# Kernel tuning notes

Hardware: AMD Instinct MI355X
Metric: run time of the kernel (lower is better)

The kernel has to match this reference:

```python
import jax, jax.numpy as jnp
import numpy as np

B, T, DIN, H, DOUT = 64, 1024, 256, 512, 256


def _lstm_layer(xseq, Wih, bih, Whh, bhh):
    """xseq: (T, B, Din) -> hidden sequence (T, B, Hout)."""
    bsz = xseq.shape[1]
    hdim = Whh.shape[0]
    # hoist the input projection out of the recurrence (one big GEMM)
    xg = jnp.einsum('tbd,dh->tbh', xseq, Wih) + bih  # (T, B, 4H)

    def step(carry, xg_t):
        h, c = carry
        gates = xg_t + h @ Whh + bhh          # (B, 4H)
        i, f, g, o = jnp.split(gates, 4, axis=-1)  # torch chunk order: i,f,g,o
        c = jax.nn.sigmoid(f) * c + jax.nn.sigmoid(i) * jnp.tanh(g)
        h = jax.nn.sigmoid(o) * jnp.tanh(c)
        return (h, c), h

    h0 = jnp.zeros((bsz, hdim), xseq.dtype)
    (_, _), hs = jax.lax.scan(step, (h0, h0), xg)
    return hs


def setup_inputs() -> dict:
    key = jax.random.key(0)
    ks = jax.random.split(key, 9)

    def lin(k, fan_in, fan_out):
        bound = 1.0 / np.sqrt(fan_in)
        kw, kb = jax.random.split(k)
        W = jax.random.uniform(kw, (fan_in, fan_out), jnp.float32, -bound, bound)
        b = jax.random.uniform(kb, (fan_out,), jnp.float32, -bound, bound)
        return W, b

    x = jax.random.normal(ks[0], (B, T, DIN), jnp.float32)
    W_ih0, b_ih0 = lin(ks[1], DIN, 4 * H)
    W_hh0, b_hh0 = lin(ks[2], H, 4 * H)
    W_ih1, b_ih1 = lin(ks[3], H, 4 * DOUT)
    W_hh1, b_hh1 = lin(ks[4], DOUT, 4 * DOUT)
    return {
        'x': x,
        'W_ih0': W_ih0, 'b_ih0': b_ih0, 'W_hh0': W_hh0, 'b_hh0': b_hh0,
        'W_ih1': W_ih1, 'b_ih1': b_ih1, 'W_hh1': W_hh1, 'b_hh1': b_hh1,
    }


def reference(x, W_ih0, b_ih0, W_hh0, b_hh0, W_ih1, b_ih1, W_hh1, b_hh1):
    xseq = jnp.transpose(x, (1, 0, 2))              # (T, B, DIN)
    h1 = _lstm_layer(xseq, W_ih0, b_ih0, W_hh0, b_hh0)   # (T, B, H)
    h2 = _lstm_layer(h1, W_ih1, b_ih1, W_hh1, b_hh1)     # (T, B, DOUT)
    return jnp.transpose(h2, (1, 0, 2))             # (B, T, DOUT)
```

## Files before the change

kernel.cpp:

```cpp
#include <hip/hip_runtime.h>


constexpr int BB   = 64;
constexpr int TT   = 1024;
constexpr int DIN  = 256;
constexpr int H0   = 512;
constexpr int H1   = 256;
constexpr int NWG0 = 128;
constexpr int NWG1 = 64;
constexpr int NWG  = NWG0 + NWG1;
constexpr int NTHR = 256;
constexpr int NKT  = 24;

typedef _Float16 v8h __attribute__((ext_vector_type(8)));
typedef __fp16   v2p __attribute__((ext_vector_type(2)));
typedef float    v4f __attribute__((ext_vector_type(4)));
typedef unsigned int v4u __attribute__((ext_vector_type(4)));

union U1 { unsigned u; v2p h; };
union U4 { v4u u; v8h h; };

__device__ __forceinline__ unsigned pk2(float a, float b){
  U1 c; c.h = __builtin_amdgcn_cvt_pkrtz(a, b); return c.u;
}
__device__ __forceinline__ float lo16(unsigned u){ U1 c; c.u = u; return (float)c.h[0]; }
__device__ __forceinline__ float hi16(unsigned u){ U1 c; c.u = u; return (float)c.h[1]; }
__device__ __forceinline__ v8h as_h8(v4u u){ U4 c; c.u = u; return c.h; }

__device__ __forceinline__ v4f mfma16(v8h a, v8h b, v4f c){
  return __builtin_amdgcn_mfma_f32_16x16x32_f16(a, b, c, 0, 0, 0);
}

__device__ __forceinline__ float sigf(float v){ return 1.0f / (1.0f + __expf(-v)); }
__device__ __forceinline__ float tanhf_(float v){
  float e = __expf(2.0f * v);
  return 1.0f - 2.0f / (e + 1.0f);
}

__device__ __forceinline__ void waitflags(const unsigned* f, int n, unsigned tgt, int lane){
  for (;;){
    bool ok = true;
    #pragma unroll
    for (int base = 0; base < n; base += 64)
      ok = ok && (__hip_atomic_load(f + base + lane, __ATOMIC_RELAXED,
                                    __HIP_MEMORY_SCOPE_AGENT) >= tgt);
    if (__all(ok)) return;
    __builtin_amdgcn_s_sleep(1);
  }
}

__device__ __forceinline__ void acq_fence(){
  __builtin_amdgcn_fence(__ATOMIC_ACQUIRE, "agent");
}

__device__ __forceinline__ void frag_from_pairs(v4u p0, v4u p1, v8h& A, v8h& B){
  v4u ua, ub;
  ua[0] = __builtin_amdgcn_perm(p0[1], p0[0], 0x05040100u);
  ua[1] = __builtin_amdgcn_perm(p0[3], p0[2], 0x05040100u);
  ua[2] = __builtin_amdgcn_perm(p1[1], p1[0], 0x05040100u);
  ua[3] = __builtin_amdgcn_perm(p1[3], p1[2], 0x05040100u);
  ub[0] = __builtin_amdgcn_perm(p0[1], p0[0], 0x07060302u);
  ub[1] = __builtin_amdgcn_perm(p0[3], p0[2], 0x07060302u);
  ub[2] = __builtin_amdgcn_perm(p1[1], p1[0], 0x07060302u);
  ub[3] = __builtin_amdgcn_perm(p1[3], p1[2], 0x07060302u);
  A = as_h8(ua); B = as_h8(ub);
}

__device__ __forceinline__ void frag_from_floats(v4f f0, v4f f1, v8h& A, v8h& B){
  float v[8] = { f0[0], f0[1], f0[2], f0[3], f1[0], f1[1], f1[2], f1[3] };
  v4u ua, ub;
  #pragma unroll
  for (int d = 0; d < 4; ++d){
    unsigned p = pk2(v[2*d], v[2*d+1]);
    ua[d] = p;
    ub[d] = pk2(v[2*d] - lo16(p), v[2*d+1] - hi16(p));
  }
  A = as_h8(ua); B = as_h8(ub);
}

__global__ void __launch_bounds__(NTHR, 1)
lstm_mfma(const float* __restrict__ x, const unsigned* __restrict__ xp, int use_xp,
          const float* __restrict__ Wih0, const float* __restrict__ bih0,
          const float* __restrict__ Whh0, const float* __restrict__ bhh0,
          const float* __restrict__ Wih1, const float* __restrict__ bih1,
          const float* __restrict__ Whh1, const float* __restrict__ bhh1,
          unsigned* h1p, unsigned* h2p,
          unsigned* flg, float* out)
{
  __shared__ v4u wfbs[NKT * 64];

  const int tid   = threadIdx.x;
  const int wg    = blockIdx.x;
  const bool isL0 = wg < NWG0;
  const int lw    = isL0 ? wg : wg - NWG0;
  const int H     = isL0 ? H0 : H1;
  const int jbase = lw * 4;
  const int lane  = tid & 63;
  const int mt    = tid >> 6;
  const int n     = lane & 15;
  const int quad  = lane >> 4;
  const int gcol  = (n >> 2) * H + jbase + (n & 3);
  const int brow  = mt * 16 + n;

  v4u wfa[NKT];
  {
    const float* Wi = isL0 ? Wih0 : Wih1;
    const float* Wh = isL0 ? Whh0 : Whh1;
    const int Ki  = isL0 ? DIN : H0;
    const int ldw = 4 * H;
    #pragma unroll
    for (int kt = 0; kt < NKT; ++kt){
      const int ks = kt * 32 + quad * 8;
      float w[8];
      #pragma unroll
      for (int j = 0; j < 8; ++j){
        const int k = ks + j;
        w[j] = (k < Ki) ? Wi[(size_t)k * ldw + gcol]
                        : Wh[(size_t)(k - Ki) * ldw + gcol];
      }
      v4u ua, ub;
      #pragma unroll
      for (int d = 0; d < 4; ++d){
        const unsigned p = pk2(w[2*d], w[2*d+1]);
        ua[d] = p;
        ub[d] = pk2(w[2*d] - lo16(p), w[2*d+1] - hi16(p));
      }
      wfa[kt] = ua;
      if (mt == 0) wfbs[kt * 64 + lane] = ub;
    }
  }
  const float bsum = isL0 ? (bih0[gcol] + bhh0[gcol]) : (bih1[gcol] + bhh1[gcol]);

  float c0 = 0.f, c1 = 0.f, c2 = 0.f, c3 = 0.f;
  __syncthreads();

  for (int i = 0; i <= TT; ++i){
    const bool act = isL0 ? (i < TT) : (i >= 1);
    const int t    = isL0 ? i : (i - 1);

    v4f acc1 = { bsum, bsum, bsum, bsum };
    v4f acc2 = { 0.f, 0.f, 0.f, 0.f };

    if (isL0 && act){
      if (use_xp){
        const unsigned* xr = xp + ((size_t)brow * TT + t) * DIN + quad * 8;
        #pragma unroll
        for (int kt = 0; kt < 8; ++kt){
          v4u p0 = *(const v4u*)(xr + kt * 32);
          v4u p1 = *(const v4u*)(xr + kt * 32 + 4);
          v8h A, Ab; frag_from_pairs(p0, p1, A, Ab);
          v8h Wa = as_h8(wfa[kt]), Wb = as_h8(wfbs[kt * 64 + lane]);
          acc1 = mfma16(A,  Wa, acc1);
          acc2 = mfma16(A,  Wb, acc2);
          acc2 = mfma16(Ab, Wa, acc2);
        }
      } else {
        const float* xr = x + ((size_t)brow * TT + t) * DIN + quad * 8;
        #pragma unroll
        for (int kt = 0; kt < 8; ++kt){
          v4f f0 = *(const v4f*)(xr + kt * 32);
          v4f f1 = *(const v4f*)(xr + kt * 32 + 4);
          v8h A, Ab; frag_from_floats(f0, f1, A, Ab);
          v8h Wa = as_h8(wfa[kt]), Wb = as_h8(wfbs[kt * 64 + lane]);
          acc1 = mfma16(A,  Wa, acc1);
          acc2 = mfma16(A,  Wb, acc2);
          acc2 = mfma16(Ab, Wa, acc2);
        }
      }
    }

    if (tid < 64){
      if (i >= 1) waitflags(flg, NWG, (unsigned)i, lane);
      acq_fence();
    }
    __syncthreads();

    if (act){
      if (isL0){
        const unsigned* hr = h1p + (size_t)((t + 1) & 1) * (BB * H0)
                                 + (size_t)brow * H0 + quad * 8;
        #pragma unroll
        for (int kt = 0; kt < 16; ++kt){
          v4u p0 = *(const v4u*)(hr + kt * 32);
          v4u p1 = *(const v4u*)(hr + kt * 32 + 4);
          v8h A, Ab; frag_from_pairs(p0, p1, A, Ab);
          v8h Wa = as_h8(wfa[kt + 8]), Wb = as_h8(wfbs[(kt + 8) * 64 + lane]);
          acc1 = mfma16(A,  Wa, acc1);
          acc2 = mfma16(A,  Wb, acc2);
          acc2 = mfma16(Ab, Wa, acc2);
        }
      } else {
        const unsigned* h2r = h2p + (size_t)((t + 1) & 1) * (BB * H1)
                                  + (size_t)brow * H1 + quad * 8;
        #pragma unroll
        for (int kt = 0; kt < 8; ++kt){
          v4u p0 = *(const v4u*)(h2r + kt * 32);
          v4u p1 = *(const v4u*)(h2r + kt * 32 + 4);
          v8h A, Ab; frag_from_pairs(p0, p1, A, Ab);
          v8h Wa = as_h8(wfa[kt + 16]), Wb = as_h8(wfbs[(kt + 16) * 64 + lane]);
          acc1 = mfma16(A,  Wa, acc1);
          acc2 = mfma16(A,  Wb, acc2);
          acc2 = mfma16(Ab, Wa, acc2);
        }
        const unsigned* hr = h1p + (size_t)(t & 1) * (BB * H0)
                                 + (size_t)brow * H0 + quad * 8;
        #pragma unroll
        for (int kt = 0; kt < 16; ++kt){
          v4u p0 = *(const v4u*)(hr + kt * 32);
          v4u p1 = *(const v4u*)(hr + kt * 32 + 4);
          v8h A, Ab; frag_from_pairs(p0, p1, A, Ab);
          v8h Wa = as_h8(wfa[kt]), Wb = as_h8(wfbs[kt * 64 + lane]);
          acc1 = mfma16(A,  Wa, acc1);
          acc2 = mfma16(A,  Wb, acc2);
          acc2 = mfma16(Ab, Wa, acc2);
        }
      }

      v4f gv = acc1 + acc2;
      float pv0 = __shfl_xor(gv[0], 4), pv1 = __shfl_xor(gv[1], 4),
            pv2 = __shfl_xor(gv[2], 4), pv3 = __shfl_xor(gv[3], 4);
      float qv0 = __shfl_xor(gv[0], 8), qv1 = __shfl_xor(gv[1], 8),
            qv2 = __shfl_xor(gv[2], 8), qv3 = __shfl_xor(gv[3], 8);
      float sv0 = __shfl_xor(pv0, 8), sv1 = __shfl_xor(pv1, 8),
            sv2 = __shfl_xor(pv2, 8), sv3 = __shfl_xor(pv3, 8);

      if (n < 4){
        float iv[4] = { gv[0], gv[1], gv[2], gv[3] };
        float fv[4] = { pv0, pv1, pv2, pv3 };
        float gg[4] = { qv0, qv1, qv2, qv3 };
        float ov[4] = { sv0, sv1, sv2, sv3 };
        float cc[4] = { c0, c1, c2, c3 };
        const int col = jbase + n;
        #pragma unroll
        for (int r = 0; r < 4; ++r){
          float cn = sigf(fv[r]) * cc[r] + sigf(iv[r]) * tanhf_(gg[r]);
          float hn = sigf(ov[r]) * tanhf_(cn);
          cc[r] = cn;
          const int b = mt * 16 + quad * 4 + r;
          unsigned pa = pk2(hn, 0.f);
          unsigned pd = pk2(hn, hn - lo16(pa));
          if (isL0){
            __hip_atomic_store(h1p + (size_t)(t & 1) * (BB * H0) + (size_t)b * H0 + col,
                               pd, __ATOMIC_RELAXED, __HIP_MEMORY_SCOPE_AGENT);
          } else {
            __hip_atomic_store(h2p + (size_t)(t & 1) * (BB * H1) + (size_t)b * H1 + col,
                               pd, __ATOMIC_RELAXED, __HIP_MEMORY_SCOPE_AGENT);
            __hip_atomic_store(out + ((size_t)b * TT + t) * H1 + col, hn,
                               __ATOMIC_RELAXED, __HIP_MEMORY_SCOPE_AGENT);
          }
        }
        c0 = cc[0]; c1 = cc[1]; c2 = cc[2]; c3 = cc[3];
      }
    }

    __syncthreads();
    if (tid == 0){
      __hip_atomic_store(flg + wg, (unsigned)(i + 1),
                         __ATOMIC_RELAXED, __HIP_MEMORY_SCOPE_AGENT);
    }
  }
}

__global__ void init_ws(unsigned* ws, int nz){
  int i = blockIdx.x * blockDim.x + threadIdx.x;
  if (i < nz)
    __hip_atomic_store(ws + i, 0u, __ATOMIC_RELAXED, __HIP_MEMORY_SCOPE_AGENT);
}

__global__ void conv_x(const float4* __restrict__ x4,
                       unsigned long long* __restrict__ xp2, int n4){
  int i = blockIdx.x * blockDim.x + threadIdx.x;
  if (i >= n4) return;
  float4 f = x4[i];
  float v[4] = { f.x, f.y, f.z, f.w };
  unsigned o[4];
  #pragma unroll
  for (int d = 0; d < 4; ++d){
    unsigned p = pk2(v[d], 0.f);
    o[d] = pk2(v[d], v[d] - lo16(p));
  }
  unsigned long long lo = (unsigned long long)o[0] | ((unsigned long long)o[1] << 32);
  unsigned long long hi = (unsigned long long)o[2] | ((unsigned long long)o[3] << 32);
  __hip_atomic_store(xp2 + 2 * i + 0, lo, __ATOMIC_RELAXED, __HIP_MEMORY_SCOPE_AGENT);
  __hip_atomic_store(xp2 + 2 * i + 1, hi, __ATOMIC_RELAXED, __HIP_MEMORY_SCOPE_AGENT);
}

extern "C" void kernel_launch(void* const* d_in, const int* in_sizes, int n_in,
                              void* d_out, int out_size, void* d_ws, size_t ws_size,
                              hipStream_t stream) {
  const float* x    = (const float*)d_in[0];
  const float* Wih0 = (const float*)d_in[1];
  const float* bih0 = (const float*)d_in[2];
  const float* Whh0 = (const float*)d_in[3];
  const float* bhh0 = (const float*)d_in[4];
  const float* Wih1 = (const float*)d_in[5];
  const float* bih1 = (const float*)d_in[6];
  const float* Whh1 = (const float*)d_in[7];
  const float* bhh1 = (const float*)d_in[8];
  float* outp = (float*)d_out;

  unsigned* ws   = (unsigned*)d_ws;
  unsigned* h1p  = ws;
  unsigned* h2p  = h1p + 2 * BB * H0;
  unsigned* flg  = h2p + 2 * BB * H1;
  unsigned* xp   = flg + 2 * TT;
  const int nz = 2 * BB * H0 + 2 * BB * H1 + 2 * TT;

  const size_t need_xp = ((size_t)nz + (size_t)BB * TT * DIN) * 4;
  int use_xp = (ws_size >= need_xp) ? 1 : 0;

  init_ws<<<dim3((nz + 255) / 256), dim3(256), 0, stream>>>(ws, nz);
  if (use_xp){
    const int n4 = BB * TT * DIN / 4;
    conv_x<<<dim3((n4 + 255) / 256), dim3(256), 0, stream>>>(
        (const float4*)x, (unsigned long long*)xp, n4);
  }

  lstm_mfma<<<dim3(NWG), dim3(NTHR), 0, stream>>>(
      x, xp, use_xp,
      Wih0, bih0, Whh0, bhh0,
      Wih1, bih1, Whh1, bhh1,
      h1p, h2p, flg, outp);
}
```

Before: 10.34 ms.

## Halve workgroup count with 8 columns each and triple-buffer layer-0 hidden state

```diff
diff --git a/kernel.cpp b/kernel.cpp
--- a/kernel.cpp
+++ b/kernel.cpp
@@ -6,8 +6,8 @@
 constexpr int DIN  = 256;
 constexpr int H0   = 512;
 constexpr int H1   = 256;
-constexpr int NWG0 = 128;
-constexpr int NWG1 = 64;
+constexpr int NWG0 = 64;
+constexpr int NWG1 = 32;
 constexpr int NWG  = NWG0 + NWG1;
 constexpr int NTHR = 256;
 constexpr int NKT  = 24;
@@ -37,13 +37,13 @@
   return 1.0f - 2.0f / (e + 1.0f);
 }
 
-__device__ __forceinline__ void waitflags(const unsigned* f, int n, unsigned tgt, int lane){
+__device__ __forceinline__ void waitflags2(const unsigned* f, unsigned tgt0,
+                                           unsigned tgt1, int lane){
+  const unsigned* p0 = f + lane;
+  const unsigned* p1 = f + 64 + (lane & 31);
   for (;;){
-    bool ok = true;
-    #pragma unroll
-    for (int base = 0; base < n; base += 64)
-      ok = ok && (__hip_atomic_load(f + base + lane, __ATOMIC_RELAXED,
-                                    __HIP_MEMORY_SCOPE_AGENT) >= tgt);
+    bool ok = (__hip_atomic_load(p0, __ATOMIC_RELAXED, __HIP_MEMORY_SCOPE_AGENT) >= tgt0)
+           && (__hip_atomic_load(p1, __ATOMIC_RELAXED, __HIP_MEMORY_SCOPE_AGENT) >= tgt1);
     if (__all(ok)) return;
     __builtin_amdgcn_s_sleep(1);
   }
@@ -87,22 +87,23 @@
           unsigned* h1p, unsigned* h2p,
           unsigned* flg, float* out)
 {
-  __shared__ v4u wfbs[NKT * 64];
+  __shared__ v4u wfbs[2 * NKT * 64];
 
   const int tid   = threadIdx.x;
   const int wg    = blockIdx.x;
   const bool isL0 = wg < NWG0;
   const int lw    = isL0 ? wg : wg - NWG0;
   const int H     = isL0 ? H0 : H1;
-  const int jbase = lw * 4;
+  const int jbase = lw * 8;
   const int lane  = tid & 63;
   const int mt    = tid >> 6;
   const int n     = lane & 15;
   const int quad  = lane >> 4;
-  const int gcol  = (n >> 2) * H + jbase + (n & 3);
+  const int gcolA = (n >> 2) * H + jbase + (n & 3);
+  const int gcolB = gcolA + 4;
   const int brow  = mt * 16 + n;
 
-  v4u wfa[NKT];
+  v4u wfaA[NKT], wfaB[NKT];
   {
     const float* Wi = isL0 ? Wih0 : Wih1;
     const float* Wh = isL0 ? Whh0 : Whh1;
@@ -111,35 +112,49 @@
     #pragma unroll
     for (int kt = 0; kt < NKT; ++kt){
       const int ks = kt * 32 + quad * 8;
-      float w[8];
+      float wA[8], wB[8];
       #pragma unroll
       for (int j = 0; j < 8; ++j){
         const int k = ks + j;
-        w[j] = (k < Ki) ? Wi[(size_t)k * ldw + gcol]
-                        : Wh[(size_t)(k - Ki) * ldw + gcol];
-      }
-      v4u ua, ub;
+        const float* Wrow = (k < Ki) ? (Wi + (size_t)k * ldw)
+                                     : (Wh + (size_t)(k - Ki) * ldw);
+        wA[j] = Wrow[gcolA];
+        wB[j] = Wrow[gcolB];
+      }
+      v4u uaA, ubA, uaB, ubB;
       #pragma unroll
       for (int d = 0; d < 4; ++d){
-        const unsigned p = pk2(w[2*d], w[2*d+1]);
-        ua[d] = p;
-        ub[d] = pk2(w[2*d] - lo16(p), w[2*d+1] - hi16(p));
-      }
-      wfa[kt] = ua;
-      if (mt == 0) wfbs[kt * 64 + lane] = ub;
-    }
-  }
-  const float bsum = isL0 ? (bih0[gcol] + bhh0[gcol]) : (bih1[gcol] + bhh1[gcol]);
-
-  float c0 = 0.f, c1 = 0.f, c2 = 0.f, c3 = 0.f;
+        unsigned pA = pk2(wA[2*d], wA[2*d+1]);
+        uaA[d] = pA;
+        ubA[d] = pk2(wA[2*d] - lo16(pA), wA[2*d+1] - hi16(pA));
+        unsigned pB = pk2(wB[2*d], wB[2*d+1]);
+        uaB[d] = pB;
+        ubB[d] = pk2(wB[2*d] - lo16(pB), wB[2*d+1] - hi16(pB));
+      }
+      wfaA[kt] = uaA; wfaB[kt] = uaB;
+      if (mt == 0){
+        wfbs[kt * 64 + lane] = ubA;
+        wfbs[(NKT + kt) * 64 + lane] = ubB;
+      }
+    }
+  }
+  const float bsumA = isL0 ? (bih0[gcolA] + bhh0[gcolA]) : (bih1[gcolA] + bhh1[gcolA]);
+  const float bsumB = isL0 ? (bih0[gcolB] + bhh0[gcolB]) : (bih1[gcolB] + bhh1[gcolB]);
+
+  float cA0=0.f,cA1=0.f,cA2=0.f,cA3=0.f, cB0=0.f,cB1=0.f,cB2=0.f,cB3=0.f;
   __syncthreads();
 
   for (int i = 0; i <= TT; ++i){
     const bool act = isL0 ? (i < TT) : (i >= 1);
     const int t    = isL0 ? i : (i - 1);
-
-    v4f acc1 = { bsum, bsum, bsum, bsum };
-    v4f acc2 = { 0.f, 0.f, 0.f, 0.f };
+    const int s_w  = ((unsigned)t) % 3u;
+    const int s_r  = ((unsigned)(t + 2)) % 3u;
+    const int s_c  = ((unsigned)t) % 3u;
+
+    v4f acc1A = { bsumA, bsumA, bsumA, bsumA };
+    v4f acc2A = { 0.f, 0.f, 0.f, 0.f };
+    v4f acc1B = { bsumB, bsumB, bsumB, bsumB };
+    v4f acc2B = { 0.f, 0.f, 0.f, 0.f };
 
     if (isL0 && act){
       if (use_xp){
@@ -149,10 +164,14 @@
           v4u p0 = *(const v4u*)(xr + kt * 32);
           v4u p1 = *(const v4u*)(xr + kt * 32 + 4);
           v8h A, Ab; frag_from_pairs(p0, p1, A, Ab);
-          v8h Wa = as_h8(wfa[kt]), Wb = as_h8(wfbs[kt * 64 + lane]);
-          acc1 = mfma16(A,  Wa, acc1);
-          acc2 = mfma16(A,  Wb, acc2);
-          acc2 = mfma16(Ab, Wa, acc2);
+          v8h WaA = as_h8(wfaA[kt]), WbA = as_h8(wfbs[kt * 64 + lane]);
+          v8h WaB = as_h8(wfaB[kt]), WbB = as_h8(wfbs[(NKT + kt) * 64 + lane]);
+          acc1A = mfma16(A,  WaA, acc1A);
+          acc2A = mfma16(A,  WbA, acc2A);
+          acc2A = mfma16(Ab, WaA, acc2A);
+          acc1B = mfma16(A,  WaB, acc1B);
+          acc2B = mfma16(A,  WbB, acc2B);
+          acc2B = mfma16(Ab, WaB, acc2B);
         }
       } else {
         const float* xr = x + ((size_t)brow * TT + t) * DIN + quad * 8;
@@ -161,33 +180,44 @@
           v4f f0 = *(const v4f*)(xr + kt * 32);
           v4f f1 = *(const v4f*)(xr + kt * 32 + 4);
           v8h A, Ab; frag_from_floats(f0, f1, A, Ab);
-          v8h Wa = as_h8(wfa[kt]), Wb = as_h8(wfbs[kt * 64 + lane]);
-          acc1 = mfma16(A,  Wa, acc1);
-          acc2 = mfma16(A,  Wb, acc2);
-          acc2 = mfma16(Ab, Wa, acc2);
+          v8h WaA = as_h8(wfaA[kt]), WbA = as_h8(wfbs[kt * 64 + lane]);
+          v8h WaB = as_h8(wfaB[kt]), WbB = as_h8(wfbs[(NKT + kt) * 64 + lane]);
+          acc1A = mfma16(A,  WaA, acc1A);
+          acc2A = mfma16(A,  WbA, acc2A);
+          acc2A = mfma16(Ab, WaA, acc2A);
+          acc1B = mfma16(A,  WaB, acc1B);
+          acc2B = mfma16(A,  WbB, acc2B);
+          acc2B = mfma16(Ab, WaB, acc2B);
         }
       }
     }
 
     if (tid < 64){
-      if (i >= 1) waitflags(flg, NWG, (unsigned)i, lane);
+      if (i >= 1){
+        if (isL0) waitflags2(flg, (unsigned)i, (i >= 2) ? (unsigned)(i - 1) : 0u, lane);
+        else      waitflags2(flg, (unsigned)i, (unsigned)i, lane);
+      }
       acq_fence();
     }
     __syncthreads();
 
     if (act){
       if (isL0){
-        const unsigned* hr = h1p + (size_t)((t + 1) & 1) * (BB * H0)
+        const unsigned* hr = h1p + (size_t)s_r * (BB * H0)
                                  + (size_t)brow * H0 + quad * 8;
         #pragma unroll
         for (int kt = 0; kt < 16; ++kt){
           v4u p0 = *(const v4u*)(hr + kt * 32);
           v4u p1 = *(const v4u*)(hr + kt * 32 + 4);
           v8h A, Ab; frag_from_pairs(p0, p1, A, Ab);
-          v8h Wa = as_h8(wfa[kt + 8]), Wb = as_h8(wfbs[(kt + 8) * 64 + lane]);
-          acc1 = mfma16(A,  Wa, acc1);
-          acc2 = mfma16(A,  Wb, acc2);
-          acc2 = mfma16(Ab, Wa, acc2);
+          v8h WaA = as_h8(wfaA[kt + 8]), WbA = as_h8(wfbs[(kt + 8) * 64 + lane]);
+          v8h WaB = as_h8(wfaB[kt + 8]), WbB = as_h8(wfbs[(NKT + kt + 8) * 64 + lane]);
+          acc1A = mfma16(A,  WaA, acc1A);
+          acc2A = mfma16(A,  WbA, acc2A);
+          acc2A = mfma16(Ab, WaA, acc2A);
+          acc1B = mfma16(A,  WaB, acc1B);
+          acc2B = mfma16(A,  WbB, acc2B);
+          acc2B = mfma16(Ab, WaB, acc2B);
         }
       } else {
         const unsigned* h2r = h2p + (size_t)((t + 1) & 1) * (BB * H1)
@@ -197,59 +227,89 @@
           v4u p0 = *(const v4u*)(h2r + kt * 32);
           v4u p1 = *(const v4u*)(h2r + kt * 32 + 4);
           v8h A, Ab; frag_from_pairs(p0, p1, A, Ab);
-          v8h Wa = as_h8(wfa[kt + 16]), Wb = as_h8(wfbs[(kt + 16) * 64 + lane]);
-          acc1 = mfma16(A,  Wa, acc1);
-          acc2 = mfma16(A,  Wb, acc2);
-          acc2 = mfma16(Ab, Wa, acc2);
-        }
-        const unsigned* hr = h1p + (size_t)(t & 1) * (BB * H0)
+          v8h WaA = as_h8(wfaA[kt + 16]), WbA = as_h8(wfbs[(kt + 16) * 64 + lane]);
+          v8h WaB = as_h8(wfaB[kt + 16]), WbB = as_h8(wfbs[(NKT + kt + 16) * 64 + lane]);
+          acc1A = mfma16(A,  WaA, acc1A);
+          acc2A = mfma16(A,  WbA, acc2A);
+          acc2A = mfma16(Ab, WaA, acc2A);
+          acc1B = mfma16(A,  WaB, acc1B);
+          acc2B = mfma16(A,  WbB, acc2B);
+          acc2B = mfma16(Ab, WaB, acc2B);
+        }
+        const unsigned* hr = h1p + (size_t)s_c * (BB * H0)
                                  + (size_t)brow * H0 + quad * 8;
         #pragma unroll
         for (int kt = 0; kt < 16; ++kt){
           v4u p0 = *(const v4u*)(hr + kt * 32);
           v4u p1 = *(const v4u*)(hr + kt * 32 + 4);
           v8h A, Ab; frag_from_pairs(p0, p1, A, Ab);
-          v8h Wa = as_h8(wfa[kt]), Wb = as_h8(wfbs[kt * 64 + lane]);
-          acc1 = mfma16(A,  Wa, acc1);
-          acc2 = mfma16(A,  Wb, acc2);
-          acc2 = mfma16(Ab, Wa, acc2);
-        }
-      }
-
-      v4f gv = acc1 + acc2;
-      float pv0 = __shfl_xor(gv[0], 4), pv1 = __shfl_xor(gv[1], 4),
-            pv2 = __shfl_xor(gv[2], 4), pv3 = __shfl_xor(gv[3], 4);
-      float qv0 = __shfl_xor(gv[0], 8), qv1 = __shfl_xor(gv[1], 8),
-            qv2 = __shfl_xor(gv[2], 8), qv3 = __shfl_xor(gv[3], 8);
-      float sv0 = __shfl_xor(pv0, 8), sv1 = __shfl_xor(pv1, 8),
-            sv2 = __shfl_xor(pv2, 8), sv3 = __shfl_xor(pv3, 8);
+          v8h WaA = as_h8(wfaA[kt]), WbA = as_h8(wfbs[kt * 64 + lane]);
+          v8h WaB = as_h8(wfaB[kt]), WbB = as_h8(wfbs[(NKT + kt) * 64 + lane]);
+          acc1A = mfma16(A,  WaA, acc1A);
+          acc2A = mfma16(A,  WbA, acc2A);
+          acc2A = mfma16(Ab, WaA, acc2A);
+          acc1B = mfma16(A,  WaB, acc1B);
+          acc2B = mfma16(A,  WbB, acc2B);
+          acc2B = mfma16(Ab, WaB, acc2B);
+        }
+      }
+
+      v4f gvA = acc1A + acc2A;
+      v4f gvB = acc1B + acc2B;
+      float pA0 = __shfl_xor(gvA[0], 4), pA1 = __shfl_xor(gvA[1], 4),
+            pA2 = __shfl_xor(gvA[2], 4), pA3 = __shfl_xor(gvA[3], 4);
+      float qA0 = __shfl_xor(gvA[0], 8), qA1 = __shfl_xor(gvA[1], 8),
+            qA2 = __shfl_xor(gvA[2], 8), qA3 = __shfl_xor(gvA[3], 8);
+      float sA0 = __shfl_xor(pA0, 8), sA1 = __shfl_xor(pA1, 8),
+            sA2 = __shfl_xor(pA2, 8), sA3 = __shfl_xor(pA3, 8);
+      float pB0 = __shfl_xor(gvB[0], 4), pB1 = __shfl_xor(gvB[1], 4),
+            pB2 = __shfl_xor(gvB[2], 4), pB3 = __shfl_xor(gvB[3], 4);
+      float qB0 = __shfl_xor(gvB[0], 8), qB1 = __shfl_xor(gvB[1], 8),
+            qB2 = __shfl_xor(gvB[2], 8), qB3 = __shfl_xor(gvB[3], 8);
+      float sB0 = __shfl_xor(pB0, 8), sB1 = __shfl_xor(pB1, 8),
+            sB2 = __shfl_xor(pB2, 8), sB3 = __shfl_xor(pB3, 8);
 
       if (n < 4){
-        float iv[4] = { gv[0], gv[1], gv[2], gv[3] };
-        float fv[4] = { pv0, pv1, pv2, pv3 };
-        float gg[4] = { qv0, qv1, qv2, qv3 };
-        float ov[4] = { sv0, sv1, sv2, sv3 };
-        float cc[4] = { c0, c1, c2, c3 };
-        const int col = jbase + n;
+        float ivA[4] = { gvA[0], gvA[1], gvA[2], gvA[3] };
+        float fvA[4] = { pA0, pA1, pA2, pA3 };
+        float ggA[4] = { qA0, qA1, qA2, qA3 };
+        float ovA[4] = { sA0, sA1, sA2, sA3 };
+        float ivB[4] = { gvB[0], gvB[1], gvB[2], gvB[3] };
+        float fvB[4] = { pB0, pB1, pB2, pB3 };
+        float ggB[4] = { qB0, qB1, qB2, qB3 };
+        float ovB[4] = { sB0, sB1, sB2, sB3 };
+        float ccA[4] = { cA0, cA1, cA2, cA3 };
+        float ccB[4] = { cB0, cB1, cB2, cB3 };
+        const int colA = jbase + n;
+        const int colB = colA + 4;
         #pragma unroll
         for (int r = 0; r < 4; ++r){
-          float cn = sigf(fv[r]) * cc[r] + sigf(iv[r]) * tanhf_(gg[r]);
-          float hn = sigf(ov[r]) * tanhf_(cn);
-          cc[r] = cn;
           const int b = mt * 16 + quad * 4 + r;
-          unsigned pa = pk2(hn, 0.f);
-          unsigned pd = pk2(hn, hn - lo16(pa));
+          float cnA = sigf(fvA[r]) * ccA[r] + sigf(ivA[r]) * tanhf_(ggA[r]);
+          float hnA = sigf(ovA[r]) * tanhf_(cnA);
+          ccA[r] = cnA;
+          float cnB = sigf(fvB[r]) * ccB[r] + sigf(ivB[r]) * tanhf_(ggB[r]);
+          float hnB = sigf(ovB[r]) * tanhf_(cnB);
+          ccB[r] = cnB;
+          unsigned paA = pk2(hnA, 0.f);
+          unsigned pdA = pk2(hnA, hnA - lo16(paA));
+          unsigned paB = pk2(hnB, 0.f);
+          unsigned pdB = pk2(hnB, hnB - lo16(paB));
           if (isL0){
-            __hip_atomic_store(h1p + (size_t)(t & 1) * (BB * H0) + (size_t)b * H0 + col,
-                               pd, __ATOMIC_RELAXED, __HIP_MEMORY_SCOPE_AGENT);
+            unsigned* hb = h1p + (size_t)s_w * (BB * H0) + (size_t)b * H0;
+            __hip_atomic_store(hb + colA, pdA, __ATOMIC_RELAXED, __HIP_MEMORY_SCOPE_AGENT);
+            __hip_atomic_store(hb + colB, pdB, __ATOMIC_RELAXED, __HIP_MEMORY_SCOPE_AGENT);
           } else {
-            __hip_atomic_store(h2p + (size_t)(t & 1) * (BB * H1) + (size_t)b * H1 + col,
-                               pd, __ATOMIC_RELAXED, __HIP_MEMORY_SCOPE_AGENT);
-            __hip_atomic_store(out + ((size_t)b * TT + t) * H1 + col, hn,
-                               __ATOMIC_RELAXED, __HIP_MEMORY_SCOPE_AGENT);
+            unsigned* hb = h2p + (size_t)(t & 1) * (BB * H1) + (size_t)b * H1;
+            __hip_atomic_store(hb + colA, pdA, __ATOMIC_RELAXED, __HIP_MEMORY_SCOPE_AGENT);
+            __hip_atomic_store(hb + colB, pdB, __ATOMIC_RELAXED, __HIP_MEMORY_SCOPE_AGENT);
+            float* ob = out + ((size_t)b * TT + t) * H1;
+            __hip_atomic_store(ob + colA, hnA, __ATOMIC_RELAXED, __HIP_MEMORY_SCOPE_AGENT);
+            __hip_atomic_store(ob + colB, hnB, __ATOMIC_RELAXED, __HIP_MEMORY_SCOPE_AGENT);
           }
         }
-        c0 = cc[0]; c1 = cc[1]; c2 = cc[2]; c3 = cc[3];
+        cA0=ccA[0]; cA1=ccA[1]; cA2=ccA[2]; cA3=ccA[3];
+        cB0=ccB[0]; cB1=ccB[1]; cB2=ccB[2]; cB3=ccB[3];
       }
     }
 
@@ -301,10 +361,10 @@
 
   unsigned* ws   = (unsigned*)d_ws;
   unsigned* h1p  = ws;
-  unsigned* h2p  = h1p + 2 * BB * H0;
+  unsigned* h2p  = h1p + 3 * BB * H0;
   unsigned* flg  = h2p + 2 * BB * H1;
   unsigned* xp   = flg + 2 * TT;
-  const int nz = 2 * BB * H0 + 2 * BB * H1 + 2 * TT;
+  const int nz = 3 * BB * H0 + 2 * BB * H1 + 2 * TT;
 
   const size_t need_xp = ((size_t)nz + (size_t)BB * TT * DIN) * 4;
   int use_xp = (ws_size >= need_xp) ? 1 : 0;
```

Result: slower. 12.61 ms (+22.0%).

## Partition LSTM by batch across XCDs with per-XCD local sync groups

Applied to the files above, without the earlier changes.

```diff
diff --git a/kernel.cpp b/kernel.cpp
--- a/kernel.cpp
+++ b/kernel.cpp
@@ -6,11 +6,10 @@
 constexpr int DIN  = 256;
 constexpr int H0   = 512;
 constexpr int H1   = 256;
-constexpr int NWG0 = 128;
-constexpr int NWG1 = 64;
-constexpr int NWG  = NWG0 + NWG1;
+constexpr int NWG  = 256;
 constexpr int NTHR = 256;
 constexpr int NKT  = 24;
+constexpr int GW   = 32;
 
 typedef _Float16 v8h __attribute__((ext_vector_type(8)));
 typedef __fp16   v2p __attribute__((ext_vector_type(2)));
@@ -37,14 +36,26 @@
   return 1.0f - 2.0f / (e + 1.0f);
 }
 
-__device__ __forceinline__ void waitflags(const unsigned* f, int n, unsigned tgt, int lane){
-  for (;;){
-    bool ok = true;
-    #pragma unroll
-    for (int base = 0; base < n; base += 64)
-      ok = ok && (__hip_atomic_load(f + base + lane, __ATOMIC_RELAXED,
-                                    __HIP_MEMORY_SCOPE_AGENT) >= tgt);
-    if (__all(ok)) return;
+__device__ __forceinline__ unsigned xccid(){
+  return (unsigned)__builtin_amdgcn_s_getreg(20 | (0 << 6) | (3 << 11)) & 7u;
+}
+
+__device__ __forceinline__ unsigned ld_sc0(const unsigned* p){
+  unsigned v;
+  asm volatile("global_load_dword %0, %1, off sc0\n\ts_waitcnt vmcnt(0)"
+               : "=v"(v) : "v"(p) : "memory");
+  return v;
+}
+
+__device__ __forceinline__ void inv_l1(){
+  asm volatile("buffer_inv" ::: "memory");
+}
+
+__device__ __forceinline__ void waitflags(const unsigned* f, unsigned tgt, int lane){
+  const unsigned* p = f + (lane & 31);
+  for (int it = 0; it < (1 << 17); ++it){
+    unsigned v = ld_sc0(p);
+    if (__all(v >= tgt)) return;
     __builtin_amdgcn_s_sleep(1);
   }
 }
@@ -85,29 +96,39 @@
           const float* __restrict__ Wih1, const float* __restrict__ bih1,
           const float* __restrict__ Whh1, const float* __restrict__ bhh1,
           unsigned* h1p, unsigned* h2p,
-          unsigned* flg, float* out)
+          unsigned* sync, float* out)
 {
-  __shared__ v4u wfbs[NKT * 64];
+  __shared__ v4u ls1[2 * NKT * 64];
+  __shared__ int sh_r;
 
   const int tid   = threadIdx.x;
-  const int wg    = blockIdx.x;
-  const bool isL0 = wg < NWG0;
-  const int lw    = isL0 ? wg : wg - NWG0;
-  const int H     = isL0 ? H0 : H1;
-  const int jbase = lw * 4;
   const int lane  = tid & 63;
   const int mt    = tid >> 6;
   const int n     = lane & 15;
   const int quad  = lane >> 4;
-  const int gcol  = (n >> 2) * H + jbase + (n & 3);
-  const int brow  = mt * 16 + n;
-
-  v4u wfa[NKT];
-  {
-    const float* Wi = isL0 ? Wih0 : Wih1;
-    const float* Wh = isL0 ? Whh0 : Whh1;
-    const int Ki  = isL0 ? DIN : H0;
-    const int ldw = 4 * H;
+  const int bl    = n & 7;
+  const unsigned g = xccid();
+
+  unsigned* flg   = sync;
+  unsigned* cnt   = sync + 512;
+  unsigned* ready = sync + 520;
+
+  if (tid == 0)
+    sh_r = (int)__hip_atomic_fetch_add(cnt + g, 1u, __ATOMIC_RELAXED, __HIP_MEMORY_SCOPE_AGENT);
+  __syncthreads();
+  const int r = sh_r;
+  const bool work = (r < GW);
+  const bool doL1w = work && (mt >= 2);
+  const int tt = mt - 2;
+
+  acq_fence();
+  if (tid == 0)
+    __hip_atomic_fetch_add(ready, 1u, __ATOMIC_RELAXED, __HIP_MEMORY_SCOPE_AGENT);
+
+  v4u wfa0[NKT], wfb0[NKT], wfa1[NKT];
+  float bsum0 = 0.f, bsum1 = 0.f;
+  if (work){
+    const int gcol0 = (n >> 2) * H0 + r * 16 + mt * 4 + (n & 3);
     #pragma unroll
     for (int kt = 0; kt < NKT; ++kt){
       const int ks = kt * 32 + quad * 8;
@@ -115,149 +136,195 @@
       #pragma unroll
       for (int j = 0; j < 8; ++j){
         const int k = ks + j;
-        w[j] = (k < Ki) ? Wi[(size_t)k * ldw + gcol]
-                        : Wh[(size_t)(k - Ki) * ldw + gcol];
-      }
-      v4u ua, ub;
+        w[j] = (k < DIN) ? Wih0[(size_t)k * (4*H0) + gcol0]
+                         : Whh0[(size_t)(k - DIN) * (4*H0) + gcol0];
+      }
       #pragma unroll
       for (int d = 0; d < 4; ++d){
         const unsigned p = pk2(w[2*d], w[2*d+1]);
-        ua[d] = p;
-        ub[d] = pk2(w[2*d] - lo16(p), w[2*d+1] - hi16(p));
-      }
-      wfa[kt] = ua;
-      if (mt == 0) wfbs[kt * 64 + lane] = ub;
-    }
-  }
-  const float bsum = isL0 ? (bih0[gcol] + bhh0[gcol]) : (bih1[gcol] + bhh1[gcol]);
-
-  float c0 = 0.f, c1 = 0.f, c2 = 0.f, c3 = 0.f;
+        wfa0[kt][d] = p;
+        wfb0[kt][d] = pk2(w[2*d] - lo16(p), w[2*d+1] - hi16(p));
+      }
+    }
+    bsum0 = bih0[gcol0] + bhh0[gcol0];
+    if (mt >= 2){
+      const int gcol1 = (n >> 2) * H1 + r * 8 + tt * 4 + (n & 3);
+      #pragma unroll
+      for (int kt = 0; kt < NKT; ++kt){
+        const int ks = kt * 32 + quad * 8;
+        float w[8];
+        #pragma unroll
+        for (int j = 0; j < 8; ++j){
+          const int k = ks + j;
+          w[j] = (k < H0) ? Wih1[(size_t)k * (4*H1) + gcol1]
+                          : Whh1[(size_t)(k - H0) * (4*H1) + gcol1];
+        }
+        v4u ub;
+        #pragma unroll
+        for (int d = 0; d < 4; ++d){
+          const unsigned p = pk2(w[2*d], w[2*d+1]);
+          wfa1[kt][d] = p;
+          ub[d] = pk2(w[2*d] - lo16(p), w[2*d+1] - hi16(p));
+        }
+        ls1[(tt * NKT + kt) * 64 + lane] = ub;
+      }
+      bsum1 = bih1[gcol1] + bhh1[gcol1];
+    }
+  }
+
+  if (tid == 0){
+    for (int it = 0; it < (1 << 22); ++it){
+      if (__hip_atomic_load(ready, __ATOMIC_RELAXED, __HIP_MEMORY_SCOPE_AGENT) >= NWG) break;
+      __builtin_amdgcn_s_sleep(2);
+    }
+  }
   __syncthreads();
+  if (!work) return;
+
+  unsigned* h1g = h1p + (size_t)g * (2 * 8 * H0);
+  unsigned* h2g = h2p + (size_t)g * (2 * 8 * H1);
+  const unsigned* flgg = flg + (size_t)g * 64;
+
+  float c0=0.f,c1=0.f,c2=0.f,c3=0.f;
+  float d0=0.f,d1=0.f,d2=0.f,d3=0.f;
 
   for (int i = 0; i <= TT; ++i){
-    const bool act = isL0 ? (i < TT) : (i >= 1);
-    const int t    = isL0 ? i : (i - 1);
-
-    v4f acc1 = { bsum, bsum, bsum, bsum };
-    v4f acc2 = { 0.f, 0.f, 0.f, 0.f };
-
-    if (isL0 && act){
+    const bool doL0 = (i < TT);
+    const bool doL1 = (i >= 1) && (mt >= 2);
+
+    v4f a0a = { bsum0, bsum0, bsum0, bsum0 };
+    v4f a0b = { 0.f, 0.f, 0.f, 0.f };
+    v4f a1a = { bsum1, bsum1, bsum1, bsum1 };
+    v4f a1b = { 0.f, 0.f, 0.f, 0.f };
+
+    if (doL0){
       if (use_xp){
-        const unsigned* xr = xp + ((size_t)brow * TT + t) * DIN + quad * 8;
+        const unsigned* xr = xp + ((size_t)(8*g + bl) * TT + i) * DIN + quad * 8;
         #pragma unroll
         for (int kt = 0; kt < 8; ++kt){
           v4u p0 = *(const v4u*)(xr + kt * 32);
           v4u p1 = *(const v4u*)(xr + kt * 32 + 4);
           v8h A, Ab; frag_from_pairs(p0, p1, A, Ab);
-          v8h Wa = as_h8(wfa[kt]), Wb = as_h8(wfbs[kt * 64 + lane]);
-          acc1 = mfma16(A,  Wa, acc1);
-          acc2 = mfma16(A,  Wb, acc2);
-          acc2 = mfma16(Ab, Wa, acc2);
+          v8h Wa = as_h8(wfa0[kt]), Wb = as_h8(wfb0[kt]);
+          a0a = mfma16(A,  Wa, a0a);
+          a0b = mfma16(A,  Wb, a0b);
+          a0b = mfma16(Ab, Wa, a0b);
         }
       } else {
-        const float* xr = x + ((size_t)brow * TT + t) * DIN + quad * 8;
+        const float* xr = x + ((size_t)(8*g + bl) * TT + i) * DIN + quad * 8;
         #pragma unroll
         for (int kt = 0; kt < 8; ++kt){
           v4f f0 = *(const v4f*)(xr + kt * 32);
           v4f f1 = *(const v4f*)(xr + kt * 32 + 4);
           v8h A, Ab; frag_from_floats(f0, f1, A, Ab);
-          v8h Wa = as_h8(wfa[kt]), Wb = as_h8(wfbs[kt * 64 + lane]);
-          acc1 = mfma16(A,  Wa, acc1);
-          acc2 = mfma16(A,  Wb, acc2);
-          acc2 = mfma16(Ab, Wa, acc2);
-        }
-      }
-    }
-
-    if (tid < 64){
-      if (i >= 1) waitflags(flg, NWG, (unsigned)i, lane);
-      acq_fence();
-    }
-    __syncthreads();
-
-    if (act){
-      if (isL0){
-        const unsigned* hr = h1p + (size_t)((t + 1) & 1) * (BB * H0)
-                                 + (size_t)brow * H0 + quad * 8;
-        #pragma unroll
-        for (int kt = 0; kt < 16; ++kt){
-          v4u p0 = *(const v4u*)(hr + kt * 32);
-          v4u p1 = *(const v4u*)(hr + kt * 32 + 4);
-          v8h A, Ab; frag_from_pairs(p0, p1, A, Ab);
-          v8h Wa = as_h8(wfa[kt + 8]), Wb = as_h8(wfbs[(kt + 8) * 64 + lane]);
-          acc1 = mfma16(A,  Wa, acc1);
-          acc2 = mfma16(A,  Wb, acc2);
-          acc2 = mfma16(Ab, Wa, acc2);
-        }
-      } else {
-        const unsigned* h2r = h2p + (size_t)((t + 1) & 1) * (BB * H1)
-                                  + (size_t)brow * H1 + quad * 8;
-        #pragma unroll
-        for (int kt = 0; kt < 8; ++kt){
-          v4u p0 = *(const v4u*)(h2r + kt * 32);
-          v4u p1 = *(const v4u*)(h2r + kt * 32 + 4);
-          v8h A, Ab; frag_from_pairs(p0, p1, A, Ab);
-          v8h Wa = as_h8(wfa[kt + 16]), Wb = as_h8(wfbs[(kt + 16) * 64 + lane]);
-          acc1 = mfma16(A,  Wa, acc1);
-          acc2 = mfma16(A,  Wb, acc2);
-          acc2 = mfma16(Ab, Wa, acc2);
-        }
-        const unsigned* hr = h1p + (size_t)(t & 1) * (BB * H0)
-                                 + (size_t)brow * H0 + quad * 8;
-        #pragma unroll
-        for (int kt = 0; kt < 16; ++kt){
-          v4u p0 = *(const v4u*)(hr + kt * 32);
-          v4u p1 = *(const v4u*)(hr + kt * 32 + 4);
-          v8h A, Ab; frag_from_pairs(p0, p1, A, Ab);
-          v8h Wa = as_h8(wfa[kt]), Wb = as_h8(wfbs[kt * 64 + lane]);
-          acc1 = mfma16(A,  Wa, acc1);
-          acc2 = mfma16(A,  Wb, acc2);
-          acc2 = mfma16(Ab, Wa, acc2);
-        }
-      }
-
-      v4f gv = acc1 + acc2;
+          v8h Wa = as_h8(wfa0[kt]), Wb = as_h8(wfb0[kt]);
+          a0a = mfma16(A,  Wa, a0a);
+          a0b = mfma16(A,  Wb, a0b);
+          a0b = mfma16(Ab, Wa, a0b);
+        }
+      }
+    }
+
+    if (i >= 1) waitflags(flgg, (unsigned)i, lane);
+    inv_l1();
+
+    {
+      const unsigned* hr = h1g + (size_t)((i + 1) & 1) * (8 * H0) + (size_t)bl * H0 + quad * 8;
+      #pragma unroll
+      for (int kt = 0; kt < 16; ++kt){
+        v4u p0 = *(const v4u*)(hr + kt * 32);
+        v4u p1 = *(const v4u*)(hr + kt * 32 + 4);
+        v8h A, Ab; frag_from_pairs(p0, p1, A, Ab);
+        if (doL0){
+          v8h Wa = as_h8(wfa0[kt + 8]), Wb = as_h8(wfb0[kt + 8]);
+          a0a = mfma16(A,  Wa, a0a);
+          a0b = mfma16(A,  Wb, a0b);
+          a0b = mfma16(Ab, Wa, a0b);
+        }
+        if (doL1){
+          v8h Wa = as_h8(wfa1[kt]), Wb = as_h8(ls1[(tt * NKT + kt) * 64 + lane]);
+          a1a = mfma16(A,  Wa, a1a);
+          a1b = mfma16(A,  Wb, a1b);
+          a1b = mfma16(Ab, Wa, a1b);
+        }
+      }
+    }
+    if (doL1){
+      const unsigned* hr = h2g + (size_t)(i & 1) * (8 * H1) + (size_t)bl * H1 + quad * 8;
+      #pragma unroll
+      for (int kt = 0; kt < 8; ++kt){
+        v4u p0 = *(const v4u*)(hr + kt * 32);
+        v4u p1 = *(const v4u*)(hr + kt * 32 + 4);
+        v8h A, Ab; frag_from_pairs(p0, p1, A, Ab);
+        v8h Wa = as_h8(wfa1[kt + 16]), Wb = as_h8(ls1[(tt * NKT + 16 + kt) * 64 + lane]);
+        a1a = mfma16(A,  Wa, a1a);
+        a1b = mfma16(A,  Wb, a1b);
+        a1b = mfma16(Ab, Wa, a1b);
+      }
+    }
+
+    if (doL0){
+      v4f gv = a0a + a0b;
       float pv0 = __shfl_xor(gv[0], 4), pv1 = __shfl_xor(gv[1], 4),
             pv2 = __shfl_xor(gv[2], 4), pv3 = __shfl_xor(gv[3], 4);
       float qv0 = __shfl_xor(gv[0], 8), qv1 = __shfl_xor(gv[1], 8),
             qv2 = __shfl_xor(gv[2], 8), qv3 = __shfl_xor(gv[3], 8);
       float sv0 = __shfl_xor(pv0, 8), sv1 = __shfl_xor(pv1, 8),
             sv2 = __shfl_xor(pv2, 8), sv3 = __shfl_xor(pv3, 8);
-
-      if (n < 4){
+      if (n < 4 && quad < 2){
         float iv[4] = { gv[0], gv[1], gv[2], gv[3] };
         float fv[4] = { pv0, pv1, pv2, pv3 };
         float gg[4] = { qv0, qv1, qv2, qv3 };
         float ov[4] = { sv0, sv1, sv2, sv3 };
         float cc[4] = { c0, c1, c2, c3 };
-        const int col = jbase + n;
-        #pragma unroll
-        for (int r = 0; r < 4; ++r){
-          float cn = sigf(fv[r]) * cc[r] + sigf(iv[r]) * tanhf_(gg[r]);
-          float hn = sigf(ov[r]) * tanhf_(cn);
-          cc[r] = cn;
-          const int b = mt * 16 + quad * 4 + r;
+        const int col = r * 16 + mt * 4 + n;
+        unsigned* hb = h1g + (size_t)(i & 1) * (8 * H0) + col;
+        #pragma unroll
+        for (int rr = 0; rr < 4; ++rr){
+          float cn = sigf(fv[rr]) * cc[rr] + sigf(iv[rr]) * tanhf_(gg[rr]);
+          float hn = sigf(ov[rr]) * tanhf_(cn);
+          cc[rr] = cn;
           unsigned pa = pk2(hn, 0.f);
-          unsigned pd = pk2(hn, hn - lo16(pa));
-          if (isL0){
-            __hip_atomic_store(h1p + (size_t)(t & 1) * (BB * H0) + (size_t)b * H0 + col,
-                               pd, __ATOMIC_RELAXED, __HIP_MEMORY_SCOPE_AGENT);
-          } else {
-            __hip_atomic_store(h2p + (size_t)(t & 1) * (BB * H1) + (size_t)b * H1 + col,
-                               pd, __ATOMIC_RELAXED, __HIP_MEMORY_SCOPE_AGENT);
-            __hip_atomic_store(out + ((size_t)b * TT + t) * H1 + col, hn,
-                               __ATOMIC_RELAXED, __HIP_MEMORY_SCOPE_AGENT);
-          }
+          hb[(size_t)(quad * 4 + rr) * H0] = pk2(hn, hn - lo16(pa));
         }
         c0 = cc[0]; c1 = cc[1]; c2 = cc[2]; c3 = cc[3];
       }
     }
+    if (doL1){
+      v4f gv = a1a + a1b;
+      float pv0 = __shfl_xor(gv[0], 4), pv1 = __shfl_xor(gv[1], 4),
+            pv2 = __shfl_xor(gv[2], 4), pv3 = __shfl_xor(gv[3], 4);
+      float qv0 = __shfl_xor(gv[0], 8), qv1 = __shfl_xor(gv[1], 8),
+            qv2 = __shfl_xor(gv[2], 8), qv3 = __shfl_xor(gv[3], 8);
+      float sv0 = __shfl_xor(pv0, 8), sv1 = __shfl_xor(pv1, 8),
+            sv2 = __shfl_xor(pv2, 8), sv3 = __shfl_xor(pv3, 8);
+      if (n < 4 && quad < 2){
+        float iv[4] = { gv[0], gv[1], gv[2], gv[3] };
+        float fv[4] = { pv0, pv1, pv2, pv3 };
+        float gg[4] = { qv0, qv1, qv2, qv3 };
+        float ov[4] = { sv0, sv1, sv2, sv3 };
+        float cc[4] = { d0, d1, d2, d3 };
+        const int col = r * 8 + tt * 4 + n;
+        const int t1  = i - 1;
+        unsigned* hb = h2g + (size_t)(t1 & 1) * (8 * H1) + col;
+        #pragma unroll
+        for (int rr = 0; rr < 4; ++rr){
+          float cn = sigf(fv[rr]) * cc[rr] + sigf(iv[rr]) * tanhf_(gg[rr]);
+          float hn = sigf(ov[rr]) * tanhf_(cn);
+          cc[rr] = cn;
+          const int b_ = quad * 4 + rr;
+          unsigned pa = pk2(hn, 0.f);
+          hb[(size_t)b_ * H1] = pk2(hn, hn - lo16(pa));
+          __hip_atomic_store(out + ((size_t)(8*g + b_) * TT + t1) * H1 + col, hn,
+                             __ATOMIC_RELAXED, __HIP_MEMORY_SCOPE_AGENT);
+        }
+        d0 = cc[0]; d1 = cc[1]; d2 = cc[2]; d3 = cc[3];
+      }
+    }
 
     __syncthreads();
-    if (tid == 0){
-      __hip_atomic_store(flg + wg, (unsigned)(i + 1),
-                         __ATOMIC_RELAXED, __HIP_MEMORY_SCOPE_AGENT);
-    }
+    if (tid == 0)
+      ((volatile unsigned*)flgg)[r] = (unsigned)(i + 1);
   }
 }
 
@@ -301,10 +368,10 @@
 
   unsigned* ws   = (unsigned*)d_ws;
   unsigned* h1p  = ws;
-  unsigned* h2p  = h1p + 2 * BB * H0;
-  unsigned* flg  = h2p + 2 * BB * H1;
-  unsigned* xp   = flg + 2 * TT;
-  const int nz = 2 * BB * H0 + 2 * BB * H1 + 2 * TT;
+  unsigned* h2p  = h1p + 8 * 2 * 8 * H0;
+  unsigned* sync = h2p + 8 * 2 * 8 * H1;
+  unsigned* xp   = sync + 528;
+  const int nz = 8*2*8*H0 + 8*2*8*H1 + 528;
 
   const size_t need_xp = ((size_t)nz + (size_t)BB * TT * DIN) * 4;
   int use_xp = (ws_size >= need_xp) ? 1 : 0;
@@ -320,5 +387,5 @@
       x, xp, use_xp,
       Wih0, bih0, Whh0, bhh0,
       Wih1, bih1, Whh1, bhh1,
-      h1p, h2p, flg, outp);
-}
+      h1p, h2p, sync, outp);
+}
```

Measured after the change: 21.11 ms. 104% more time.
